# Kernel tuning notes

Hardware: AMD Instinct MI355X
Metric: run time of the kernel (lower is better)

## Reference

```python
import jax, jax.numpy as jnp
import numpy as np

N, E, D_IN, D, HEADS = 8192, 2048, 256, 256, 4
EPS = 1e-5
NEG = -1e9  # large negative instead of -inf (rows guaranteed non-empty anyway)


def _layernorm(x, g, b):
    mu = jnp.mean(x, axis=-1, keepdims=True)
    var = jnp.mean(jnp.square(x - mu), axis=-1, keepdims=True)
    return (x - mu) * jax.lax.rsqrt(var + EPS) * g + b


def _mha(q_x, kv_x, in_w, in_b, out_w, out_b, mask):
    """torch nn.MultiheadAttention (batch=1, eval) with boolean attn_mask.
    q_x: [Lq, D], kv_x: [Lk, D], mask: [Lq, Lk] True = blocked."""
    hd = D // HEADS
    wq, wk, wv = jnp.split(in_w, 3, axis=0)   # each [D, D]
    bq, bk, bv = jnp.split(in_b, 3, axis=0)
    q = (q_x @ wq.T + bq).reshape(-1, HEADS, hd).transpose(1, 0, 2)  # [h, Lq, hd]
    k = (kv_x @ wk.T + bk).reshape(-1, HEADS, hd).transpose(1, 0, 2)
    v = (kv_x @ wv.T + bv).reshape(-1, HEADS, hd).transpose(1, 0, 2)
    scores = jnp.einsum('hqd,hkd->hqk', q, k) / jnp.sqrt(jnp.asarray(hd, q.dtype))
    scores = jnp.where(mask[None, :, :], NEG, scores)
    attn = jax.nn.softmax(scores, axis=-1)
    out = jnp.einsum('hqk,hkd->hqd', attn, v)           # [h, Lq, hd]
    out = out.transpose(1, 0, 2).reshape(-1, D)          # [Lq, D]
    return out @ out_w.T + out_b


def setup_inputs() -> dict:
    key = jax.random.key(0)
    ks = jax.random.split(key, 12)
    s = 0.02
    x_0 = jax.random.normal(ks[0], (N, D_IN), jnp.float32)
    x_1 = jax.random.normal(ks[1], (E, D_IN), jnp.float32)
    H = (jax.random.uniform(ks[2], (N, E)) < 0.01).astype(jnp.float32)
    H = H.at[jnp.arange(N), jnp.arange(N) % E].set(1.0)
    return {
        'x_0': x_0, 'x_1': x_1, 'incidence_1': H,
        'node_w': jax.random.normal(ks[3], (D, D_IN), jnp.float32) * s,
        'node_b': jnp.zeros((D,), jnp.float32),
        'edge_w': jax.random.normal(ks[4], (D, D_IN), jnp.float32) * s,
        'edge_b': jnp.zeros((D,), jnp.float32),
        'n2e_in_w': jax.random.normal(ks[5], (3 * D, D), jnp.float32) * s,
        'n2e_in_b': jnp.zeros((3 * D,), jnp.float32),
        'n2e_out_w': jax.random.normal(ks[6], (D, D), jnp.float32) * s,
        'n2e_out_b': jnp.zeros((D,), jnp.float32),
        'e2n_in_w': jax.random.normal(ks[7], (3 * D, D), jnp.float32) * s,
        'e2n_in_b': jnp.zeros((3 * D,), jnp.float32),
        'e2n_out_w': jax.random.normal(ks[8], (D, D), jnp.float32) * s,
        'e2n_out_b': jnp.zeros((D,), jnp.float32),
        'norm1_g': jnp.ones((D,), jnp.float32),
        'norm1_b': jnp.zeros((D,), jnp.float32),
        'norm2_g': jnp.ones((D,), jnp.float32),
        'norm2_b': jnp.zeros((D,), jnp.float32),
    }


def reference(x_0, x_1, incidence_1, node_w, node_b, edge_w, edge_b,
              n2e_in_w, n2e_in_b, n2e_out_w, n2e_out_b,
              e2n_in_w, e2n_in_b, e2n_out_w, e2n_out_b,
              norm1_g, norm1_b, norm2_g, norm2_b):
    H = incidence_1                      # [N, E]
    x_0_p = x_0 @ node_w.T + node_b      # [N, D]
    x_1_p = x_1 @ edge_w.T + edge_b      # [E, D]
    # node -> edge: edges query nodes, mask where H.T == 0
    x_1_u = _mha(x_1_p, x_0_p, n2e_in_w, n2e_in_b, n2e_out_w, n2e_out_b,
                 H.T == 0)
    x_1_u = _layernorm(x_1_p + x_1_u, norm1_g, norm1_b)
    # edge -> node: nodes query updated edges, mask where H == 0
    x_0_u = _mha(x_0_p, x_1_u, e2n_in_w, e2n_in_b, e2n_out_w, e2n_out_b,
                 H == 0)
    x_0_u = _layernorm(x_0_p + x_0_u, norm2_g, norm2_b)
    return (x_0_u, x_1_u)
```

## Files before the change

kernel.cpp:

```cpp
#include <hip/hip_runtime.h>
#include <hip/hip_bf16.h>

using bf16 = __hip_bfloat16;
typedef __attribute__((ext_vector_type(4))) float  f32x4;
typedef __attribute__((ext_vector_type(8))) short  s16x8;

#define QSTRIDE 1040
#define ASTRIDE 520
#define BSTRIDE 2064
#define CMAX 256
#define RMAX 128

struct ConvDesc { const float* src[14]; int dstoff[14]; int cnt[14]; };

__global__ __launch_bounds__(256)
void conv_weights(ConvDesc d, bf16* __restrict__ dst, int* __restrict__ cz, int czn)
{
    const int seg = blockIdx.x >> 6;
    const int blk = blockIdx.x & 63;
    if (seg == 14) {
        for (int i = blk * 256 + threadIdx.x; i < czn; i += 64 * 256)
            cz[i] = 0;
        return;
    }
    const float* __restrict__ s = d.src[seg];
    bf16* __restrict__ o = dst + d.dstoff[seg];
    const int n = d.cnt[seg];
    for (int i = blk * 256 + threadIdx.x; i < n; i += 64 * 256)
        o[i] = __float2bfloat16(s[i]);
}

__global__ __launch_bounds__(256)
void build_lists(const float* __restrict__ H, int* __restrict__ col_cnt,
                 unsigned short* __restrict__ col_idx, int* __restrict__ row_cnt,
                 unsigned short* __restrict__ row_idx)
{
    __shared__ int rc;
    const int t = threadIdx.x;

    int n = blockIdx.x;
    const float* Hp = H + (size_t)n * 2048 + t * 8;
    f32x4 c0 = *(const f32x4*)Hp;
    f32x4 c1 = *(const f32x4*)(Hp + 4);

    while (n < 8192) {
        const int nn = n + 1024;
        f32x4 p0, p1;
        if (nn < 8192) {
            const float* Hq = H + (size_t)nn * 2048 + t * 8;
            p0 = *(const f32x4*)Hq;
            p1 = *(const f32x4*)(Hq + 4);
        }

        if (t == 0) rc = 0;
        __syncthreads();

        float hv[8];
#pragma unroll
        for (int j = 0; j < 4; j++) { hv[j] = c0[j]; hv[4 + j] = c1[j]; }

#pragma unroll
        for (int j = 0; j < 8; j++) {
            if (hv[j] != 0.f) {
                const int e = t * 8 + j;
                const int sr = atomicAdd(&rc, 1);
                if (sr < RMAX) row_idx[(size_t)n * RMAX + sr] = (unsigned short)e;
                const int sc = atomicAdd(&col_cnt[e], 1);
                if (sc < CMAX) col_idx[(size_t)e * CMAX + sc] = (unsigned short)n;
            }
        }
        __syncthreads();
        if (t == 0) row_cnt[n] = (rc < RMAX) ? rc : RMAX;

        n = nn; c0 = p0; c1 = p1;
    }
}

__global__ __launch_bounds__(256, 2)
void gemm_proj(const float* __restrict__ X0, const float* __restrict__ X1,
               const bf16* __restrict__ Wc, const bf16* __restrict__ biasc,
               bf16* __restrict__ outB)
{
    __shared__ __align__(16) bf16 As[4 * QSTRIDE];
    __shared__ __align__(16) bf16 Bs[4 * QSTRIDE];

    const int t    = threadIdx.x;
    const int lane = t & 63;
    const int w    = t >> 6;
    const int wm   = (w >> 1) * 64;
    const int wn   = (w & 1) * 64;
    const int bt   = blockIdx.x >> 1;
    const int tn   = (blockIdx.x & 1) * 128;
    if (bt >= 80) return;

    const float* __restrict__ A = (bt < 64) ? X0 : X1;
    const int arow = (bt < 64) ? bt * 128 : (bt - 64) * 128;
    const bf16* __restrict__ W    = Wc    + ((bt < 64) ? 0 : 65536);
    const bf16* __restrict__ bias = biasc + ((bt < 64) ? 0 : 256);
    const int tm = bt * 128;

    f32x4 acc[4][4];
#pragma unroll
    for (int i = 0; i < 4; i++)
#pragma unroll
        for (int j = 0; j < 4; j++)
#pragma unroll
            for (int r = 0; r < 4; r++) acc[i][j][r] = 0.f;

    const int m0 = t >> 2,         q0 = t & 3;
    const int m1 = (t + 256) >> 2, q1 = (t + 256) & 3;
    const int fq = lane >> 4, fr = lane & 15;

    for (int k0 = 0; k0 < 256; k0 += 32) {
        f32x4 a0l = *(const f32x4*)(A + (size_t)(arow + m0) * 256 + k0 + q0 * 8);
        f32x4 a0h = *(const f32x4*)(A + (size_t)(arow + m0) * 256 + k0 + q0 * 8 + 4);
        f32x4 a1l = *(const f32x4*)(A + (size_t)(arow + m1) * 256 + k0 + q1 * 8);
        f32x4 a1h = *(const f32x4*)(A + (size_t)(arow + m1) * 256 + k0 + q1 * 8 + 4);
        union { s16x8 v; bf16 e[8]; } u0, u1;
#pragma unroll
        for (int j = 0; j < 4; j++) {
            u0.e[j] = __float2bfloat16(a0l[j]); u0.e[4 + j] = __float2bfloat16(a0h[j]);
            u1.e[j] = __float2bfloat16(a1l[j]); u1.e[4 + j] = __float2bfloat16(a1h[j]);
        }
        s16x8 sb0 = *(const s16x8*)(W + (size_t)(tn + m0) * 256 + k0 + q0 * 8);
        s16x8 sb1 = *(const s16x8*)(W + (size_t)(tn + m1) * 256 + k0 + q1 * 8);

        __syncthreads();
        *(s16x8*)&As[q0 * QSTRIDE + m0 * 8] = u0.v;
        *(s16x8*)&As[q1 * QSTRIDE + m1 * 8] = u1.v;
        *(s16x8*)&Bs[q0 * QSTRIDE + m0 * 8] = sb0;
        *(s16x8*)&Bs[q1 * QSTRIDE + m1 * 8] = sb1;
        __syncthreads();

        s16x8 af[4], bfv[4];
#pragma unroll
        for (int i = 0; i < 4; i++) {
            af[i]  = *(const s16x8*)&As[fq * QSTRIDE + (wm + i * 16 + fr) * 8];
            bfv[i] = *(const s16x8*)&Bs[fq * QSTRIDE + (wn + i * 16 + fr) * 8];
        }
#pragma unroll
        for (int i = 0; i < 4; i++)
#pragma unroll
            for (int j = 0; j < 4; j++)
                acc[i][j] = __builtin_amdgcn_mfma_f32_16x16x32_bf16(
                    af[i], bfv[j], acc[i][j], 0, 0, 0);
    }

#pragma unroll
    for (int j = 0; j < 4; j++) {
        const int ncol = tn + wn + j * 16 + fr;
        const float bj = __bfloat162float(bias[ncol]);
#pragma unroll
        for (int i = 0; i < 4; i++)
#pragma unroll
            for (int r = 0; r < 4; r++) {
                const int mrow = tm + wm + i * 16 + fq * 4 + r;
                outB[(size_t)mrow * 256 + ncol] = __float2bfloat16(acc[i][j][r] + bj);
            }
    }
}

__global__ __launch_bounds__(256, 2)
void gemm_dual(const bf16* __restrict__ A0, const bf16* __restrict__ W0,
               const bf16* __restrict__ bias0, bf16* __restrict__ out0,
               int N0, int tiles0, int nblk0,
               const bf16* __restrict__ A1, const bf16* __restrict__ W1,
               const bf16* __restrict__ bias1, bf16* __restrict__ out1,
               int N1, int tiles1)
{
    __shared__ __align__(16) bf16 As[4 * QSTRIDE];
    __shared__ __align__(16) bf16 Bs[4 * QSTRIDE];

    const int t    = threadIdx.x;
    const int lane = t & 63;
    const int w    = t >> 6;
    const int wm   = (w >> 1) * 64;
    const int wn   = (w & 1) * 64;

    const bool second = (blockIdx.x >= (unsigned)nblk0);
    const int  bi     = second ? (blockIdx.x - nblk0) : blockIdx.x;
    const bf16* __restrict__ A    = second ? A1 : A0;
    const bf16* __restrict__ W    = second ? W1 : W0;
    const bf16* __restrict__ bias = second ? bias1 : bias0;
    bf16* __restrict__ outB       = second ? out1 : out0;
    const int N      = second ? N1 : N0;
    const int tilesN = second ? tiles1 : tiles0;
    const int tm = (bi / tilesN) * 128;
    const int tn = (bi % tilesN) * 128;

    f32x4 acc[4][4];
#pragma unroll
    for (int i = 0; i < 4; i++)
#pragma unroll
        for (int j = 0; j < 4; j++)
#pragma unroll
            for (int r = 0; r < 4; r++) acc[i][j][r] = 0.f;

    const int m0 = t >> 2,         q0 = t & 3;
    const int m1 = (t + 256) >> 2, q1 = (t + 256) & 3;
    const int fq = lane >> 4, fr = lane & 15;

    for (int k0 = 0; k0 < 256; k0 += 32) {
        s16x8 sa0 = *(const s16x8*)(A + (size_t)(tm + m0) * 256 + k0 + q0 * 8);
        s16x8 sa1 = *(const s16x8*)(A + (size_t)(tm + m1) * 256 + k0 + q1 * 8);
        s16x8 sb0 = *(const s16x8*)(W + (size_t)(tn + m0) * 256 + k0 + q0 * 8);
        s16x8 sb1 = *(const s16x8*)(W + (size_t)(tn + m1) * 256 + k0 + q1 * 8);

        __syncthreads();
        *(s16x8*)&As[q0 * QSTRIDE + m0 * 8] = sa0;
        *(s16x8*)&As[q1 * QSTRIDE + m1 * 8] = sa1;
        *(s16x8*)&Bs[q0 * QSTRIDE + m0 * 8] = sb0;
        *(s16x8*)&Bs[q1 * QSTRIDE + m1 * 8] = sb1;
        __syncthreads();

        s16x8 af[4], bfv[4];
#pragma unroll
        for (int i = 0; i < 4; i++) {
            af[i]  = *(const s16x8*)&As[fq * QSTRIDE + (wm + i * 16 + fr) * 8];
            bfv[i] = *(const s16x8*)&Bs[fq * QSTRIDE + (wn + i * 16 + fr) * 8];
        }
#pragma unroll
        for (int i = 0; i < 4; i++)
#pragma unroll
            for (int j = 0; j < 4; j++)
                acc[i][j] = __builtin_amdgcn_mfma_f32_16x16x32_bf16(
                    af[i], bfv[j], acc[i][j], 0, 0, 0);
    }

#pragma unroll
    for (int j = 0; j < 4; j++) {
        const int ncol = tn + wn + j * 16 + fr;
        const float bj = __bfloat162float(bias[ncol]);
#pragma unroll
        for (int i = 0; i < 4; i++)
#pragma unroll
            for (int r = 0; r < 4; r++) {
                const int mrow = tm + wm + i * 16 + fq * 4 + r;
                outB[(size_t)mrow * N + ncol] = __float2bfloat16(acc[i][j][r] + bj);
            }
    }
}

__global__ __launch_bounds__(256, 2)
void gemm_ln(const bf16* __restrict__ A, const bf16* __restrict__ W,
             const float* __restrict__ biasF, const bf16* __restrict__ xp,
             const float* __restrict__ g, const float* __restrict__ b,
             float* __restrict__ outF, bf16* __restrict__ outB)
{
    __shared__ __align__(16) bf16 As[4 * ASTRIDE];
    __shared__ __align__(16) bf16 Bs[4 * BSTRIDE];
    __shared__ float rs1[64], rs2[64];

    const int t    = threadIdx.x;
    const int lane = t & 63;
    const int w    = t >> 6;
    const int fq   = lane >> 4;
    const int fr   = lane & 15;
    const int tm   = blockIdx.x * 64;

    if (t < 64) { rs1[t] = 0.f; rs2[t] = 0.f; }

    f32x4 acc[4][4];
#pragma unroll
    for (int i = 0; i < 4; i++)
#pragma unroll
        for (int j = 0; j < 4; j++)
#pragma unroll
            for (int r = 0; r < 4; r++) acc[i][j][r] = 0.f;

    const int mA = t >> 2, qA = t & 3;

    for (int k0 = 0; k0 < 256; k0 += 32) {
        s16x8 sa = *(const s16x8*)(A + (size_t)(tm + mA) * 256 + k0 + qA * 8);
        s16x8 sb[4];
#pragma unroll
        for (int s = 0; s < 4; s++)
            sb[s] = *(const s16x8*)(W + (size_t)(mA + 64 * s) * 256 + k0 + qA * 8);

        __syncthreads();
        *(s16x8*)&As[qA * ASTRIDE + mA * 8] = sa;
#pragma unroll
        for (int s = 0; s < 4; s++)
            *(s16x8*)&Bs[qA * BSTRIDE + (mA + 64 * s) * 8] = sb[s];
        __syncthreads();

        s16x8 af[4], bfv[4];
#pragma unroll
        for (int i = 0; i < 4; i++) {
            af[i]  = *(const s16x8*)&As[fq * ASTRIDE + (i * 16 + fr) * 8];
            bfv[i] = *(const s16x8*)&Bs[fq * BSTRIDE + (w * 64 + i * 16 + fr) * 8];
        }
#pragma unroll
        for (int i = 0; i < 4; i++)
#pragma unroll
            for (int j = 0; j < 4; j++)
                acc[i][j] = __builtin_amdgcn_mfma_f32_16x16x32_bf16(
                    af[i], bfv[j], acc[i][j], 0, 0, 0);
    }

    float bj[4], gj[4], bbj[4];
    int colv[4];
#pragma unroll
    for (int j = 0; j < 4; j++) {
        colv[j] = w * 64 + j * 16 + fr;
        bj[j]  = biasF[colv[j]];
        gj[j]  = g[colv[j]];
        bbj[j] = b[colv[j]];
    }

#pragma unroll
    for (int i = 0; i < 4; i++) {
#pragma unroll
        for (int r = 0; r < 4; r++) {
            const int row = i * 16 + fq * 4 + r;
            float t1 = 0.f, t2 = 0.f;
#pragma unroll
            for (int j = 0; j < 4; j++) {
                float v = acc[i][j][r] + bj[j]
                        + __bfloat162float(xp[(size_t)(tm + row) * 256 + colv[j]]);
                acc[i][j][r] = v;
                t1 += v;
                t2 += v * v;
            }
#pragma unroll
            for (int o = 1; o < 16; o <<= 1) {
                t1 += __shfl_xor(t1, o);
                t2 += __shfl_xor(t2, o);
            }
            if (fr == 0) {
                atomicAdd(&rs1[row], t1);
                atomicAdd(&rs2[row], t2);
            }
        }
    }
    __syncthreads();

#pragma unroll
    for (int i = 0; i < 4; i++) {
#pragma unroll
        for (int r = 0; r < 4; r++) {
            const int row = i * 16 + fq * 4 + r;
            const float mu  = rs1[row] * (1.f / 256.f);
            const float var = rs2[row] * (1.f / 256.f) - mu * mu;
            const float rstd = rsqrtf(var + 1e-5f);
#pragma unroll
            for (int j = 0; j < 4; j++) {
                const float y = (acc[i][j][r] - mu) * rstd * gj[j] + bbj[j];
                outF[(size_t)(tm + row) * 256 + colv[j]] = y;
                if (outB) outB[(size_t)(tm + row) * 256 + colv[j]] = __float2bfloat16(y);
            }
        }
    }
}

__global__ __launch_bounds__(256)
void sparse_attn(const bf16* __restrict__ Q, int qs,
                 const bf16* __restrict__ Kb, const bf16* __restrict__ Vb, int kvs,
                 const int* __restrict__ cnts, const unsigned short* __restrict__ idx,
                 int lmax, int idxmask, bf16* __restrict__ out)
{
    __shared__ float sc[4][CMAX];
    __shared__ unsigned short nls[CMAX];
    const int qi   = blockIdx.x;
    const int h    = threadIdx.x >> 6;
    const int lane = threadIdx.x & 63;
    const int grp  = lane >> 3;
    const int sub  = lane & 7;

    int n = cnts[qi];
    if (n > lmax) n = lmax;

    if (h == 0)
        for (int i = lane; i < n; i += 64)
            nls[i] = (unsigned short)(((int)idx[(size_t)qi * lmax + i]) & idxmask);
    __syncthreads();

    if (n <= 0) {
        out[(size_t)qi * 256 + h * 64 + lane] = __float2bfloat16(0.f);
        return;
    }

    float qv[8];
    {
        union { f32x4 v; unsigned short u[8]; } qu;
        qu.v = *(const f32x4*)(Q + (size_t)qi * qs + h * 64 + sub * 8);
#pragma unroll
        for (int j = 0; j < 8; j++)
            qv[j] = __uint_as_float(((unsigned)qu.u[j]) << 16) * 0.125f;
    }

    float mx = -1e30f;
#pragma unroll 2
    for (int base = 0; base < n; base += 8) {
        const int i = base + grp;
        float s = -1e30f;
        if (i < n) {
            const int nb = nls[i];
            union { f32x4 v; unsigned short u[8]; } ku;
            ku.v = *(const f32x4*)(Kb + (size_t)nb * kvs + h * 64 + sub * 8);
            float a = 0.f;
#pragma unroll
            for (int j = 0; j < 8; j++)
                a += __uint_as_float(((unsigned)ku.u[j]) << 16) * qv[j];
            a += __shfl_xor(a, 1);
            a += __shfl_xor(a, 2);
            a += __shfl_xor(a, 4);
            if (sub == 0) sc[h][i] = a;
            s = a;
        }
        mx = fmaxf(mx, s);
    }
#pragma unroll
    for (int o = 32; o > 0; o >>= 1) mx = fmaxf(mx, __shfl_xor(mx, o));

    float sum = 0.f;
    for (int base = 0; base < n; base += 64) {
        const int i = base + lane;
        if (i < n) {
            const float p = __expf(sc[h][i] - mx);
            sc[h][i] = p;
            sum += p;
        }
    }
#pragma unroll
    for (int o = 32; o > 0; o >>= 1) sum += __shfl_xor(sum, o);
    const float inv = 1.f / sum;

    float oa[8];
#pragma unroll
    for (int j = 0; j < 8; j++) oa[j] = 0.f;
#pragma unroll 2
    for (int base = 0; base < n; base += 8) {
        const int i = base + grp;
        if (i < n) {
            const float p = sc[h][i];
            const int nb = nls[i];
            union { f32x4 v; unsigned short u[8]; } vu;
            vu.v = *(const f32x4*)(Vb + (size_t)nb * kvs + h * 64 + sub * 8);
#pragma unroll
            for (int j = 0; j < 8; j++)
                oa[j] += p * __uint_as_float(((unsigned)vu.u[j]) << 16);
        }
    }
#pragma unroll
    for (int j = 0; j < 8; j++) {
        oa[j] += __shfl_xor(oa[j], 8);
        oa[j] += __shfl_xor(oa[j], 16);
        oa[j] += __shfl_xor(oa[j], 32);
    }
    if (grp == 0) {
        union { s16x8 v; bf16 e[8]; } ou;
#pragma unroll
        for (int j = 0; j < 8; j++) ou.e[j] = __float2bfloat16(oa[j] * inv);
        *(s16x8*)(out + (size_t)qi * 256 + h * 64 + sub * 8) = ou.v;
    }
}

extern "C" void kernel_launch(void* const* d_in, const int* in_sizes, int n_in,
                              void* d_out, int out_size, void* d_ws, size_t ws_size,
                              hipStream_t stream)
{
    const int N = 8192, E = 2048;

    float* out0 = (float*)d_out;
    float* out1 = (float*)d_out + (size_t)N * 256;

    char* wp = (char*)d_ws;
    auto carve = [&](size_t bytes) { void* p = wp; wp += (bytes + 15) & ~size_t(15); return p; };

    bf16*  wcat    = (bf16*)          carve(657408 * 2);
    int*   col_cnt = (int*)           carve((size_t)E * 4);
    int*   row_cnt = (int*)           carve((size_t)N * 4);
    unsigned short* col_idx = (unsigned short*)carve((size_t)E * CMAX * 2);
    unsigned short* row_idx = (unsigned short*)carve((size_t)N * RMAX * 2);
    bf16*  xp01    = (bf16*) carve((size_t)(N + E) * 256 * 2);
    bf16*  kvq     = (bf16*) carve((size_t)N * 768 * 2);
    bf16*  q1      = (bf16*) carve((size_t)E * 256 * 2);
    bf16*  attn1   = (bf16*) carve((size_t)E * 256 * 2);
    bf16*  x1u_b   = (bf16*) carve((size_t)E * 256 * 2);
    bf16*  kv2     = (bf16*) carve((size_t)E * 512 * 2);
    bf16*  attn2   = (bf16*) carve((size_t)N * 256 * 2);

    bf16* x0p = xp01;
    bf16* x1p = xp01 + (size_t)N * 256;

    const int O_PW   = 0;
    const int O_PB   = 131072;
    const int O_KVQ  = 131584;
    const int O_KVQB = 328192;
    const int O_Q1W  = 328960;
    const int O_Q1B  = 394496;
    const int O_KV2W = 394752;
    const int O_KV2B = 525824;
    const int O_O1W  = 526336;
    const int O_O2W  = 591872;

    ConvDesc cd;
    const float* srcs[14] = {
        (const float*)d_in[3], (const float*)d_in[5],
        (const float*)d_in[4], (const float*)d_in[6],
        (const float*)d_in[7] + 65536, (const float*)d_in[11],
        (const float*)d_in[8] + 256,   (const float*)d_in[12],
        (const float*)d_in[7],         (const float*)d_in[8],
        (const float*)d_in[11] + 65536,(const float*)d_in[12] + 256,
        (const float*)d_in[9],         (const float*)d_in[13]
    };
    const int offs[14] = {O_PW, O_PW + 65536, O_PB, O_PB + 256,
                          O_KVQ, O_KVQ + 131072, O_KVQB, O_KVQB + 512,
                          O_Q1W, O_Q1B, O_KV2W, O_KV2B, O_O1W, O_O2W};
    const int cnts[14] = {65536, 65536, 256, 256, 131072, 65536, 512, 256,
                          65536, 256, 131072, 512, 65536, 65536};
    for (int i = 0; i < 14; i++) { cd.src[i] = srcs[i]; cd.dstoff[i] = offs[i]; cd.cnt[i] = cnts[i]; }

    conv_weights<<<15 * 64, 256, 0, stream>>>(cd, wcat, col_cnt, E);

    build_lists<<<1024, 256, 0, stream>>>((const float*)d_in[2], col_cnt, col_idx,
                                          row_cnt, row_idx);

    gemm_proj<<<160, 256, 0, stream>>>((const float*)d_in[0], (const float*)d_in[1],
                                       wcat + O_PW, wcat + O_PB, xp01);

    gemm_dual<<<384 + 32, 256, 0, stream>>>(x0p, wcat + O_KVQ, wcat + O_KVQB, kvq,
                                            768, 6, 384,
                                            x1p, wcat + O_Q1W, wcat + O_Q1B, q1,
                                            256, 2);

    sparse_attn<<<E, 256, 0, stream>>>(q1, 256, kvq, kvq + 256, 768,
                                       col_cnt, col_idx, CMAX, N - 1, attn1);
    gemm_ln<<<E / 64, 256, 0, stream>>>(attn1, wcat + O_O1W, (const float*)d_in[10],
                                        x1p, (const float*)d_in[15], (const float*)d_in[16],
                                        out1, x1u_b);

    gemm_dual<<<64, 256, 0, stream>>>(x1u_b, wcat + O_KV2W, wcat + O_KV2B, kv2,
                                      512, 4, 64,
                                      nullptr, nullptr, nullptr, nullptr, 256, 2);
    sparse_attn<<<N, 256, 0, stream>>>(kvq + 512, 768, kv2, kv2 + 256, 512,
                                       row_cnt, row_idx, RMAX, E - 1, attn2);
    gemm_ln<<<N / 64, 256, 0, stream>>>(attn2, wcat + O_O2W, (const float*)d_in[14],
                                        x0p, (const float*)d_in[17], (const float*)d_in[18],
                                        out0, nullptr);
}
```

Before: 267.5 us.

## Fuse incidence list building into projection GEMM launch and pad column counters

Merges the build_lists kernel into the input-projection GEMM as extra blocks of a single launch. The list-building blocks and GEMM tiles can then run concurrently, and one launch boundary goes away. Column-count atomics are spread across a 16-int stride so each counter sits on its own 64-byte line, which is meant to cut contention between counters that would otherwise share cache lines. The costs are a larger counter buffer and zeroing, plus LDS and launch bounds shared between two unrelated workloads.

```diff
diff --git a/kernel.cpp b/kernel.cpp
--- a/kernel.cpp
+++ b/kernel.cpp
@@ -10,6 +10,7 @@
 #define BSTRIDE 2064
 #define CMAX 256
 #define RMAX 128
+#define CSTRIDE 16
 
 struct ConvDesc { const float* src[14]; int dstoff[14]; int cnt[14]; };
 
@@ -30,61 +31,60 @@
         o[i] = __float2bfloat16(s[i]);
 }
 
-__global__ __launch_bounds__(256)
-void build_lists(const float* __restrict__ H, int* __restrict__ col_cnt,
-                 unsigned short* __restrict__ col_idx, int* __restrict__ row_cnt,
-                 unsigned short* __restrict__ row_idx)
-{
-    __shared__ int rc;
-    const int t = threadIdx.x;
-
-    int n = blockIdx.x;
-    const float* Hp = H + (size_t)n * 2048 + t * 8;
-    f32x4 c0 = *(const f32x4*)Hp;
-    f32x4 c1 = *(const f32x4*)(Hp + 4);
-
-    while (n < 8192) {
-        const int nn = n + 1024;
-        f32x4 p0, p1;
-        if (nn < 8192) {
-            const float* Hq = H + (size_t)nn * 2048 + t * 8;
-            p0 = *(const f32x4*)Hq;
-            p1 = *(const f32x4*)(Hq + 4);
-        }
-
-        if (t == 0) rc = 0;
-        __syncthreads();
-
-        float hv[8];
-#pragma unroll
-        for (int j = 0; j < 4; j++) { hv[j] = c0[j]; hv[4 + j] = c1[j]; }
-
-#pragma unroll
-        for (int j = 0; j < 8; j++) {
-            if (hv[j] != 0.f) {
-                const int e = t * 8 + j;
-                const int sr = atomicAdd(&rc, 1);
-                if (sr < RMAX) row_idx[(size_t)n * RMAX + sr] = (unsigned short)e;
-                const int sc = atomicAdd(&col_cnt[e], 1);
-                if (sc < CMAX) col_idx[(size_t)e * CMAX + sc] = (unsigned short)n;
-            }
-        }
-        __syncthreads();
-        if (t == 0) row_cnt[n] = (rc < RMAX) ? rc : RMAX;
-
-        n = nn; c0 = p0; c1 = p1;
-    }
-}
-
 __global__ __launch_bounds__(256, 2)
-void gemm_proj(const float* __restrict__ X0, const float* __restrict__ X1,
-               const bf16* __restrict__ Wc, const bf16* __restrict__ biasc,
-               bf16* __restrict__ outB)
+void proj_lists(const float* __restrict__ X0, const float* __restrict__ X1,
+                const bf16* __restrict__ Wc, const bf16* __restrict__ biasc,
+                bf16* __restrict__ outB,
+                const float* __restrict__ H, int* __restrict__ col_cnt,
+                unsigned short* __restrict__ col_idx, int* __restrict__ row_cnt,
+                unsigned short* __restrict__ row_idx)
 {
     __shared__ __align__(16) bf16 As[4 * QSTRIDE];
     __shared__ __align__(16) bf16 Bs[4 * QSTRIDE];
-
-    const int t    = threadIdx.x;
+    __shared__ int rc;
+
+    const int t = threadIdx.x;
+
+    if (blockIdx.x >= 160) {
+        int n = blockIdx.x - 160;
+        const float* Hp = H + (size_t)n * 2048 + t * 8;
+        f32x4 c0 = *(const f32x4*)Hp;
+        f32x4 c1 = *(const f32x4*)(Hp + 4);
+
+        while (n < 8192) {
+            const int nn = n + 1024;
+            f32x4 p0, p1;
+            if (nn < 8192) {
+                const float* Hq = H + (size_t)nn * 2048 + t * 8;
+                p0 = *(const f32x4*)Hq;
+                p1 = *(const f32x4*)(Hq + 4);
+            }
+
+            if (t == 0) rc = 0;
+            __syncthreads();
+
+            float hv[8];
+#pragma unroll
+            for (int j = 0; j < 4; j++) { hv[j] = c0[j]; hv[4 + j] = c1[j]; }
+
+#pragma unroll
+            for (int j = 0; j < 8; j++) {
+                if (hv[j] != 0.f) {
+                    const int e = t * 8 + j;
+                    const int sr = atomicAdd(&rc, 1);
+                    if (sr < RMAX) row_idx[(size_t)n * RMAX + sr] = (unsigned short)e;
+                    const int sc = atomicAdd(&col_cnt[e * CSTRIDE], 1);
+                    if (sc < CMAX) col_idx[(size_t)e * CMAX + sc] = (unsigned short)n;
+                }
+            }
+            __syncthreads();
+            if (t == 0) row_cnt[n] = (rc < RMAX) ? rc : RMAX;
+
+            n = nn; c0 = p0; c1 = p1;
+        }
+        return;
+    }
+
     const int lane = t & 63;
     const int w    = t >> 6;
     const int wm   = (w >> 1) * 64;
@@ -356,7 +356,8 @@
 __global__ __launch_bounds__(256)
 void sparse_attn(const bf16* __restrict__ Q, int qs,
                  const bf16* __restrict__ Kb, const bf16* __restrict__ Vb, int kvs,
-                 const int* __restrict__ cnts, const unsigned short* __restrict__ idx,
+                 const int* __restrict__ cnts, int cstride,
+                 const unsigned short* __restrict__ idx,
                  int lmax, int idxmask, bf16* __restrict__ out)
 {
     __shared__ float sc[4][CMAX];
@@ -367,7 +368,7 @@
     const int grp  = lane >> 3;
     const int sub  = lane & 7;
 
-    int n = cnts[qi];
+    int n = cnts[(size_t)qi * cstride];
     if (n > lmax) n = lmax;
 
     if (h == 0)
@@ -469,7 +470,7 @@
     auto carve = [&](size_t bytes) { void* p = wp; wp += (bytes + 15) & ~size_t(15); return p; };
 
     bf16*  wcat    = (bf16*)          carve(657408 * 2);
-    int*   col_cnt = (int*)           carve((size_t)E * 4);
+    int*   col_cnt = (int*)           carve((size_t)E * CSTRIDE * 4);
     int*   row_cnt = (int*)           carve((size_t)N * 4);
     unsigned short* col_idx = (unsigned short*)carve((size_t)E * CMAX * 2);
     unsigned short* row_idx = (unsigned short*)carve((size_t)N * RMAX * 2);
@@ -512,13 +513,12 @@
                           65536, 256, 131072, 512, 65536, 65536};
     for (int i = 0; i < 14; i++) { cd.src[i] = srcs[i]; cd.dstoff[i] = offs[i]; cd.cnt[i] = cnts[i]; }
 
-    conv_weights<<<15 * 64, 256, 0, stream>>>(cd, wcat, col_cnt, E);
-
-    build_lists<<<1024, 256, 0, stream>>>((const float*)d_in[2], col_cnt, col_idx,
-                                          row_cnt, row_idx);
-
-    gemm_proj<<<160, 256, 0, stream>>>((const float*)d_in[0], (const float*)d_in[1],
-                                       wcat + O_PW, wcat + O_PB, xp01);
+    conv_weights<<<15 * 64, 256, 0, stream>>>(cd, wcat, col_cnt, E * CSTRIDE);
+
+    proj_lists<<<160 + 1024, 256, 0, stream>>>(
+        (const float*)d_in[0], (const float*)d_in[1],
+        wcat + O_PW, wcat + O_PB, xp01,
+        (const float*)d_in[2], col_cnt, col_idx, row_cnt, row_idx);
 
     gemm_dual<<<384 + 32, 256, 0, stream>>>(x0p, wcat + O_KVQ, wcat + O_KVQB, kvq,
                                             768, 6, 384,
@@ -526,7 +526,7 @@
                                             256, 2);
 
     sparse_attn<<<E, 256, 0, stream>>>(q1, 256, kvq, kvq + 256, 768,
-                                       col_cnt, col_idx, CMAX, N - 1, attn1);
+                                       col_cnt, CSTRIDE, col_idx, CMAX, N - 1, attn1);
     gemm_ln<<<E / 64, 256, 0, stream>>>(attn1, wcat + O_O1W, (const float*)d_in[10],
                                         x1p, (const float*)d_in[15], (const float*)d_in[16],
                                         out1, x1u_b);
@@ -535,7 +535,7 @@
                                       512, 4, 64,
                                       nullptr, nullptr, nullptr, nullptr, 256, 2);
     sparse_attn<<<N, 256, 0, stream>>>(kvq + 512, 768, kv2, kv2 + 256, 512,
-                                       row_cnt, row_idx, RMAX, E - 1, attn2);
+                                       row_cnt, 1, row_idx, RMAX, E - 1, attn2);
     gemm_ln<<<N / 64, 256, 0, stream>>>(attn2, wcat + O_O2W, (const float*)d_in[14],
                                         x0p, (const float*)d_in[17], (const float*)d_in[18],
                                         out0, nullptr);
```

After: 277.1 us. 1.04x slower.
